# Performance work log

Measured on AMD Instinct MI355X. Metric: run time of the kernel, lower is better.

The kernel has to match this reference:

```python
import jax, jax.numpy as jnp
import numpy as np

FFT_LEN = 256
WIN_LEN = 768
FRM_LEN = 128
PPF_TAP = WIN_LEN // FFT_LEN  # 6
SCALE = -256.0
GROUP_DELAY = 648  # module uses group_delay = -648
B, C, S, T = 8, 2, FFT_LEN // 2 + 1, 4096


def _make_lpf(win_len):
    # firwin(win_len, 0.5, window='hann', scale=False) equivalent
    n = np.arange(win_len, dtype=np.float64)
    w = 0.5 - 0.5 * np.cos(2.0 * np.pi * n / (win_len - 1))
    h = w * np.sinc(0.5 * (n - (win_len - 1) / 2.0))
    return jnp.asarray(h, dtype=jnp.float32)


def setup_inputs() -> dict:
    key = jax.random.key(0)
    k1, k2 = jax.random.split(key)
    spectrum_real = jax.random.normal(k1, (B, C, S, T), dtype=jnp.float32)
    spectrum_imag = jax.random.normal(k2, (B, C, S, T), dtype=jnp.float32)
    lpf_coef = _make_lpf(WIN_LEN)
    return {"spectrum_real": spectrum_real, "spectrum_imag": spectrum_imag, "lpf_coef": lpf_coef}


def reference(spectrum_real, spectrum_imag, lpf_coef):
    # spectrum: (B, C, S, T) complex; per-frame irfft over subbands
    spec = jnp.swapaxes(spectrum_real + 1j * spectrum_imag, -1, -2)  # (B,C,T,S)
    fftout = jnp.fft.irfft(spec, n=FFT_LEN, axis=-1)                 # (B,C,T,FFT_LEN)
    rev = fftout[..., ::-1]                                          # comp_in[fft_len-j-1]
    v = jnp.tile(rev, (1, 1, 1, PPF_TAP)) * lpf_coef                 # (B,C,T,WIN_LEN)
    b, c, t, _ = v.shape
    num_samples = t * FRM_LEN
    # overlap-add: frame t contributes v[t] at offset t*FRM_LEN (shifting buffer recurrence)
    idx = jnp.arange(t)[:, None] * FRM_LEN + jnp.arange(WIN_LEN)[None, :]  # (T, WIN_LEN)
    y = jnp.zeros((b, c, num_samples + WIN_LEN), dtype=v.dtype)
    y = y.at[..., idx].add(v)[..., :num_samples]
    y = y * (FRM_LEN * SCALE)
    # circular shift by group delay, then trim the wrapped tail
    y = jnp.roll(y, -GROUP_DELAY, axis=-1)[..., :-GROUP_DELAY]
    return y
```

## Files before the change

### kernel.cpp

```cpp
#include <hip/hip_runtime.h>
#include <hip/hip_bf16.h>
#include <math.h>

#define NBINS   129
#define NFFT    256
#define WINL    768
#define TFRAMES 4096
#define OUTL    523640
#define NQUADS  (OUTL / 4)
#define SHIFT   648
#define WSEG    26
#define CHUNK   (WSEG * 128)
#define NCHUNK  ((OUTL + CHUNK - 1) / CHUNK)
#define FF      64
#define FFS     32

#define KDIM    288
#define KROW    296
#define GROW    268
#define WBYTES  (16 * 9 * 64 * 16)
#define GBYTES  ((size_t)16 * TFRAMES * 256 * 2)
#define NSTG    17

typedef __attribute__((ext_vector_type(8))) short bf16x8;
typedef __attribute__((ext_vector_type(4))) float f32x4;

static __device__ __forceinline__ ushort f2bf(float x) {
    union { float f; unsigned u; } v; v.f = x;
    unsigned r = v.u + 0x7FFFu + ((v.u >> 16) & 1u);
    return (ushort)(r >> 16);
}
static __device__ __forceinline__ float bf2f(ushort u) {
    union { unsigned u_; float f; } g; g.u_ = ((unsigned)u) << 16; return g.f;
}

__global__ void build_w_kernel(ushort* __restrict__ wp)
{
    const int gid  = blockIdx.x * 256 + threadIdx.x;
    const int lane = gid & 63;
    const int mtks = gid >> 6;
    const int ks   = mtks % 9;
    const int mt   = mtks / 9;
    const int m    = mt * 16 + (lane & 15);
    const int kb   = ks * 32 + ((lane >> 4) << 3);

    ushort o[8];
    #pragma unroll
    for (int e = 0; e < 8; ++e) {
        const int kap = kb + e;
        float val = 0.f;
        if (kap < 258) {
            const int k = kap >> 1;
            float s, c;
            sincospif((float)(k * (m + 1)) * (1.0f / 128.0f), &s, &c);
            if (kap & 1)  val = (k >= 1 && k <= 127) ? s * (2.0f / 256.0f) : 0.f;
            else          val = (k == 0 || k == 128) ? c * (1.0f / 256.0f)
                                                     : c * (2.0f / 256.0f);
        }
        o[e] = f2bf(val);
    }
    int4 pk;
    pk.x = o[0] | (o[1] << 16); pk.y = o[2] | (o[3] << 16);
    pk.z = o[4] | (o[5] << 16); pk.w = o[6] | (o[7] << 16);
    ((int4*)wp)[gid] = pk;
}

__global__ __launch_bounds__(256, 3)
void pfb_dft_kernel(const float* __restrict__ gre, const float* __restrict__ gim,
                    const ushort* __restrict__ wp, ushort* __restrict__ Gg)
{
    const int t0  = blockIdx.x * FF;
    const int bc  = blockIdx.y;
    const int tid = threadIdx.x;
    const int lane = tid & 63;
    const int wid  = tid >> 6;
    const int brow = lane & 15;
    const int kq   = lane >> 4;
    const size_t specBase = (size_t)bc * NBINS * TFRAMES;
    const float* __restrict__ reB = gre + specBase + t0;
    const float* __restrict__ imB = gim + specBase + t0;

    f32x4 acc[4][4];
    #pragma unroll
    for (int mi = 0; mi < 4; ++mi)
        #pragma unroll
        for (int nt = 0; nt < 4; ++nt)
            acc[mi][nt] = (f32x4){0.f, 0.f, 0.f, 0.f};

    const ushort* wbase0 = wp + ((size_t)(wid * 4) * 9 * 64 + (size_t)lane) * 8;

    #pragma unroll
    for (int ks = 0; ks < 9; ++ks) {
        const int k0 = ks * 16 + kq * 4;
        bf16x8 aw[4];
        #pragma unroll
        for (int mi = 0; mi < 4; ++mi)
            aw[mi] = *(const bf16x8*)(wbase0 + mi * 4608 + ks * 512);

        bf16x8 bv[4];
        #pragma unroll
        for (int nt = 0; nt < 4; ++nt) {
            const int t = nt * 16 + brow;
            union { bf16x8 v; unsigned u[4]; } pk;
            #pragma unroll
            for (int j = 0; j < 4; ++j) {
                const int k = (k0 + j <= 128) ? (k0 + j) : 128;
                const size_t off = (size_t)k * TFRAMES + (size_t)t;
                const float re = reB[off];
                const float im = imB[off];
                __hip_bfloat162 p = __float22bfloat162_rn(make_float2(re, im));
                pk.u[j] = *(unsigned*)&p;
            }
            bv[nt] = pk.v;
        }

        #pragma unroll
        for (int mi = 0; mi < 4; ++mi)
            #pragma unroll
            for (int nt = 0; nt < 4; ++nt)
                acc[mi][nt] = __builtin_amdgcn_mfma_f32_16x16x32_bf16(aw[mi], bv[nt], acc[mi][nt], 0, 0, 0);
    }

    ushort* gout = Gg + ((size_t)bc * TFRAMES + t0) * NFFT;
    #pragma unroll
    for (int mi = 0; mi < 4; ++mi) {
        const int m0 = (wid * 4 + mi) * 16 + (kq << 2);
        #pragma unroll
        for (int nt = 0; nt < 4; ++nt) {
            const int f = nt * 16 + brow;
            __hip_bfloat162 lo = __float22bfloat162_rn(make_float2(acc[mi][nt].x, acc[mi][nt].y));
            __hip_bfloat162 hi = __float22bfloat162_rn(make_float2(acc[mi][nt].z, acc[mi][nt].w));
            uint2 pk; pk.x = *(unsigned*)&lo; pk.y = *(unsigned*)&hi;
            *(uint2*)&gout[f * NFFT + m0] = pk;
        }
    }
}

__global__ __launch_bounds__(256, 8)
void pfb_oa_kernel(const ushort* __restrict__ Gg, const float* __restrict__ glpf,
                   float* __restrict__ out)
{
    const int tid = threadIdx.x;
    const int bc  = blockIdx.y;
    const int h0  = blockIdx.x * 512 + tid;

    const int b = (4 * h0 + SHIFT) & 127;
    float4 lw[6];
    #pragma unroll
    for (int p = 0; p < 6; ++p) lw[p] = *(const float4*)&glpf[(p << 7) + b];

    const ushort* Gb = Gg + (size_t)bc * TFRAMES * NFFT;
    const size_t outBase = (size_t)bc * OUTL;

    #pragma unroll
    for (int j = 0; j < 2; ++j) {
        const int h = h0 + j * 256;
        int a = (4 * h + SHIFT) >> 7;
        if (a > TFRAMES - 1) a = TFRAMES - 1;
        float s0 = 0.f, s1 = 0.f, s2 = 0.f, s3 = 0.f;
        #pragma unroll
        for (int p = 0; p < 6; ++p) {
            const ushort4 q = *(const ushort4*)&Gb[(size_t)(a - p) * NFFT + b + ((p & 1) << 7)];
            s0 += lw[p].x * bf2f(q.x);
            s1 += lw[p].y * bf2f(q.y);
            s2 += lw[p].z * bf2f(q.z);
            s3 += lw[p].w * bf2f(q.w);
        }
        if (h < NQUADS) {
            float4 o;
            o.x = s0 * (-32768.0f); o.y = s1 * (-32768.0f);
            o.z = s2 * (-32768.0f); o.w = s3 * (-32768.0f);
            *(float4*)&out[outBase + 4 * h] = o;
        }
    }
}

__global__ __launch_bounds__(256, 4)
void pfb_mfma_kernel(const float* __restrict__ gre, const float* __restrict__ gim,
                     const float* __restrict__ glpf, const ushort* __restrict__ wp,
                     float* __restrict__ out)
{
    __shared__ ushort s_bufu[FFS * KROW];
    __shared__ float  s_lpf[WINL];
    ushort* s_Bu = s_bufu;
    ushort (*s_G)[GROW] = (ushort (*)[GROW])s_bufu;

    const int q   = blockIdx.x;
    const int bc  = blockIdx.y;
    const int tid = threadIdx.x;
    const int t0  = WSEG * q;
    const size_t specBase = (size_t)bc * NBINS * TFRAMES;

    for (int idx = tid; idx < WINL; idx += 256) s_lpf[idx] = glpf[idx];

    float vr[NSTG], vi[NSTG];
    #pragma unroll
    for (int r = 0; r < NSTG; ++r) {
        const int idx = tid + r * 256;
        const int k = idx >> 5, f = idx & 31;
        const int t = t0 + f;
        const bool ok = (idx < NBINS * FFS) && (t < TFRAMES);
        float a = 0.f, bb = 0.f;
        if (ok) {
            const size_t g = specBase + (size_t)k * TFRAMES + (size_t)t;
            a = gre[g]; bb = gim[g];
        }
        vr[r] = a; vi[r] = bb;
    }
    #pragma unroll
    for (int r = 0; r < NSTG; ++r) {
        const int idx = tid + r * 256;
        if (idx < NBINS * FFS) {
            const int k = idx >> 5, f = idx & 31;
            __hip_bfloat162 p = __float22bfloat162_rn(make_float2(vr[r], vi[r]));
            *(__hip_bfloat162*)&s_Bu[f * KROW + 2 * k] = p;
        }
    }
    for (int idx = tid; idx < FFS * (KROW - 258); idx += 256) {
        const int f = idx / (KROW - 258), r = idx - f * (KROW - 258);
        s_Bu[f * KROW + 258 + r] = 0;
    }
    __syncthreads();

    const int lane = tid & 63;
    const int wid  = tid >> 6;
    const int brow = lane & 15;
    const int kgrp = (lane >> 4) << 3;

    bf16x8 bfrag[2][9];
    #pragma unroll
    for (int nt = 0; nt < 2; ++nt)
        #pragma unroll
        for (int ks = 0; ks < 9; ++ks)
            bfrag[nt][ks] = *(const bf16x8*)&s_Bu[(nt * 16 + brow) * KROW + ks * 32 + kgrp];

    f32x4 acc[4][2];
    #pragma unroll
    for (int mi = 0; mi < 4; ++mi)
        #pragma unroll
        for (int nt = 0; nt < 2; ++nt)
            acc[mi][nt] = (f32x4){0.f, 0.f, 0.f, 0.f};

    #pragma unroll 1
    for (int mi = 0; mi < 4; ++mi) {
        const ushort* wbase = wp + ((size_t)((wid * 4 + mi) * 9) * 64 + lane) * 8;
        #pragma unroll
        for (int ks = 0; ks < 9; ++ks) {
            const bf16x8 aw = *(const bf16x8*)(wbase + ks * 512);
            acc[mi][0] = __builtin_amdgcn_mfma_f32_16x16x32_bf16(aw, bfrag[0][ks], acc[mi][0], 0, 0, 0);
            acc[mi][1] = __builtin_amdgcn_mfma_f32_16x16x32_bf16(aw, bfrag[1][ks], acc[mi][1], 0, 0, 0);
        }
    }
    __syncthreads();

    #pragma unroll
    for (int mi = 0; mi < 4; ++mi) {
        const int m0 = (wid * 4 + mi) * 16 + ((lane >> 4) << 2);
        #pragma unroll
        for (int nt = 0; nt < 2; ++nt) {
            const int f = nt * 16 + brow;
            __hip_bfloat162 lo = __float22bfloat162_rn(make_float2(acc[mi][nt].x, acc[mi][nt].y));
            __hip_bfloat162 hi = __float22bfloat162_rn(make_float2(acc[mi][nt].z, acc[mi][nt].w));
            uint2 pk; pk.x = *(unsigned*)&lo; pk.y = *(unsigned*)&hi;
            *(uint2*)&s_G[f][m0] = pk;
        }
    }
    __syncthreads();

    const size_t outBase = (size_t)bc * OUTL;
    const int i0 = q * CHUNK;
    #pragma unroll 1
    for (int r = 0; r < 13; ++r) {
        const int i = i0 + r * 256 + tid;
        const int s = i + SHIFT;
        const int tlo = (s - 640) >> 7;
        int thi = s >> 7;
        if (thi > t0 + FFS - 1) thi = t0 + FFS - 1;
        if (thi > TFRAMES - 1) thi = TFRAMES - 1;
        float sum = 0.f;
        #pragma unroll
        for (int u = 0; u < 6; ++u) {
            const int t  = tlo + u;
            int jj = s - (t << 7);
            if (jj < 0) jj = 0;
            const float w = s_lpf[jj];
            sum += (t <= thi) ? w * bf2f(s_G[t - t0][jj & 255]) : 0.f;
        }
        if (i < OUTL) out[outBase + i] = sum * (-32768.0f);
    }
}

extern "C" void kernel_launch(void* const* d_in, const int* in_sizes, int n_in,
                              void* d_out, int out_size, void* d_ws, size_t ws_size,
                              hipStream_t stream)
{
    const float* gre  = (const float*)d_in[0];
    const float* gim  = (const float*)d_in[1];
    const float* glpf = (const float*)d_in[2];
    float* out = (float*)d_out;

    if (ws_size >= (size_t)WBYTES + GBYTES) {
        ushort* wp = (ushort*)d_ws;
        ushort* Gg = (ushort*)((char*)d_ws + WBYTES);
        build_w_kernel<<<36, 256, 0, stream>>>(wp);
        dim3 gridA(TFRAMES / FF, 16);
        pfb_dft_kernel<<<gridA, 256, 0, stream>>>(gre, gim, wp, Gg);
        dim3 gridB((NQUADS + 511) / 512, 16);
        pfb_oa_kernel<<<gridB, 256, 0, stream>>>(Gg, glpf, out);
    } else if (ws_size >= (size_t)WBYTES) {
        ushort* wp = (ushort*)d_ws;
        build_w_kernel<<<36, 256, 0, stream>>>(wp);
        dim3 grid(NCHUNK, 16);
        pfb_mfma_kernel<<<grid, 256, 0, stream>>>(gre, gim, glpf, wp, out);
    }
}
```

Measured before the change: 54.59 us.

## Restructure DFT GEMM so each wave owns 16 frames staged through LDS

```diff
diff --git a/kernel.cpp b/kernel.cpp
--- a/kernel.cpp
+++ b/kernel.cpp
@@ -12,11 +12,12 @@
 #define WSEG    26
 #define CHUNK   (WSEG * 128)
 #define NCHUNK  ((OUTL + CHUNK - 1) / CHUNK)
-#define FF      64
+#define FPW     16
 #define FFS     32
 
 #define KDIM    288
 #define KROW    296
+#define GROWL   264
 #define GROW    268
 #define WBYTES  (16 * 9 * 64 * 16)
 #define GBYTES  ((size_t)16 * TFRAMES * 256 * 2)
@@ -65,74 +66,80 @@
     ((int4*)wp)[gid] = pk;
 }
 
-__global__ __launch_bounds__(256, 3)
-void pfb_dft_kernel(const float* __restrict__ gre, const float* __restrict__ gim,
-                    const ushort* __restrict__ wp, ushort* __restrict__ Gg)
-{
-    const int t0  = blockIdx.x * FF;
-    const int bc  = blockIdx.y;
-    const int tid = threadIdx.x;
+__global__ __launch_bounds__(256, 4)
+void pfb_dft_wave_kernel(const float* __restrict__ gre, const float* __restrict__ gim,
+                         const ushort* __restrict__ wp, ushort* __restrict__ Gg)
+{
+    __shared__ ushort s_mem[4][FPW * KROW];
+
+    const int tid  = threadIdx.x;
+    const int wave = tid >> 6;
     const int lane = tid & 63;
-    const int wid  = tid >> 6;
-    const int brow = lane & 15;
-    const int kq   = lane >> 4;
+    const int bc   = blockIdx.y;
+    const int t0   = (blockIdx.x * 4 + wave) * FPW;
+    ushort* sl = s_mem[wave];
     const size_t specBase = (size_t)bc * NBINS * TFRAMES;
     const float* __restrict__ reB = gre + specBase + t0;
     const float* __restrict__ imB = gim + specBase + t0;
 
-    f32x4 acc[4][4];
-    #pragma unroll
-    for (int mi = 0; mi < 4; ++mi)
-        #pragma unroll
-        for (int nt = 0; nt < 4; ++nt)
-            acc[mi][nt] = (f32x4){0.f, 0.f, 0.f, 0.f};
-
-    const ushort* wbase0 = wp + ((size_t)(wid * 4) * 9 * 64 + (size_t)lane) * 8;
-
-    #pragma unroll
-    for (int ks = 0; ks < 9; ++ks) {
-        const int k0 = ks * 16 + kq * 4;
-        bf16x8 aw[4];
-        #pragma unroll
-        for (int mi = 0; mi < 4; ++mi)
-            aw[mi] = *(const bf16x8*)(wbase0 + mi * 4608 + ks * 512);
-
-        bf16x8 bv[4];
-        #pragma unroll
-        for (int nt = 0; nt < 4; ++nt) {
-            const int t = nt * 16 + brow;
-            union { bf16x8 v; unsigned u[4]; } pk;
+    #pragma unroll
+    for (int it = 0; it < 9; ++it) {
+        const int idx = lane + it * 64;
+        if (idx < NBINS * 4) {
+            const int k = idx >> 2, f4 = idx & 3;
+            const float4 a = *(const float4*)&reB[(size_t)k * TFRAMES + 4 * f4];
+            const float4 b = *(const float4*)&imB[(size_t)k * TFRAMES + 4 * f4];
+            const float rr[4] = {a.x, a.y, a.z, a.w};
+            const float ii[4] = {b.x, b.y, b.z, b.w};
             #pragma unroll
             for (int j = 0; j < 4; ++j) {
-                const int k = (k0 + j <= 128) ? (k0 + j) : 128;
-                const size_t off = (size_t)k * TFRAMES + (size_t)t;
-                const float re = reB[off];
-                const float im = imB[off];
-                __hip_bfloat162 p = __float22bfloat162_rn(make_float2(re, im));
-                pk.u[j] = *(unsigned*)&p;
+                __hip_bfloat162 p = __float22bfloat162_rn(make_float2(rr[j], ii[j]));
+                *(__hip_bfloat162*)&sl[(4 * f4 + j) * KROW + 2 * k] = p;
             }
-            bv[nt] = pk.v;
-        }
-
-        #pragma unroll
-        for (int mi = 0; mi < 4; ++mi)
-            #pragma unroll
-            for (int nt = 0; nt < 4; ++nt)
-                acc[mi][nt] = __builtin_amdgcn_mfma_f32_16x16x32_bf16(aw[mi], bv[nt], acc[mi][nt], 0, 0, 0);
+        }
+    }
+    #pragma unroll
+    for (int it = 0; it < 5; ++it) {
+        const int idx = lane + it * 64;
+        if (idx < FPW * 19) {
+            const int f = idx / 19, w = idx - f * 19;
+            *(unsigned*)&sl[f * KROW + 258 + 2 * w] = 0u;
+        }
+    }
+
+    const int brow = lane & 15;
+    const int kq   = lane >> 4;
+
+    f32x4 acc[16];
+    #pragma unroll
+    for (int mt = 0; mt < 16; ++mt) acc[mt] = (f32x4){0.f, 0.f, 0.f, 0.f};
+
+    const ushort* wl = wp + (size_t)lane * 8;
+    #pragma unroll
+    for (int ks = 0; ks < 9; ++ks) {
+        const bf16x8 bv = *(const bf16x8*)&sl[brow * KROW + ks * 32 + (kq << 3)];
+        #pragma unroll
+        for (int mt = 0; mt < 16; ++mt) {
+            const bf16x8 aw = *(const bf16x8*)(wl + ((size_t)(mt * 9 + ks) << 9));
+            acc[mt] = __builtin_amdgcn_mfma_f32_16x16x32_bf16(aw, bv, acc[mt], 0, 0, 0);
+        }
+    }
+
+    #pragma unroll
+    for (int mt = 0; mt < 16; ++mt) {
+        const int m0 = mt * 16 + (kq << 2);
+        __hip_bfloat162 lo = __float22bfloat162_rn(make_float2(acc[mt].x, acc[mt].y));
+        __hip_bfloat162 hi = __float22bfloat162_rn(make_float2(acc[mt].z, acc[mt].w));
+        uint2 pk; pk.x = *(unsigned*)&lo; pk.y = *(unsigned*)&hi;
+        *(uint2*)&sl[brow * GROWL + m0] = pk;
     }
 
     ushort* gout = Gg + ((size_t)bc * TFRAMES + t0) * NFFT;
     #pragma unroll
-    for (int mi = 0; mi < 4; ++mi) {
-        const int m0 = (wid * 4 + mi) * 16 + (kq << 2);
-        #pragma unroll
-        for (int nt = 0; nt < 4; ++nt) {
-            const int f = nt * 16 + brow;
-            __hip_bfloat162 lo = __float22bfloat162_rn(make_float2(acc[mi][nt].x, acc[mi][nt].y));
-            __hip_bfloat162 hi = __float22bfloat162_rn(make_float2(acc[mi][nt].z, acc[mi][nt].w));
-            uint2 pk; pk.x = *(unsigned*)&lo; pk.y = *(unsigned*)&hi;
-            *(uint2*)&gout[f * NFFT + m0] = pk;
-        }
+    for (int it = 0; it < 8; ++it) {
+        const int c = lane + it * 64;
+        const int row = c >> 5, chunk = c & 31;
+        *(bf16x8*)&gout[c * 8] = *(const bf16x8*)&sl[row * GROWL + chunk * 8];
     }
 }
 
@@ -303,8 +310,8 @@
         ushort* wp = (ushort*)d_ws;
         ushort* Gg = (ushort*)((char*)d_ws + WBYTES);
         build_w_kernel<<<36, 256, 0, stream>>>(wp);
-        dim3 gridA(TFRAMES / FF, 16);
-        pfb_dft_kernel<<<gridA, 256, 0, stream>>>(gre, gim, wp, Gg);
+        dim3 gridA(TFRAMES / (4 * FPW), 16);
+        pfb_dft_wave_kernel<<<gridA, 256, 0, stream>>>(gre, gim, wp, Gg);
         dim3 gridB((NQUADS + 511) / 512, 16);
         pfb_oa_kernel<<<gridB, 256, 0, stream>>>(Gg, glpf, out);
     } else if (ws_size >= (size_t)WBYTES) {
```

Result: slower. 72.29 us (+32.4%).
